# Optimization experiments

Hardware: AMD Instinct MI355X
Metric: run time of the kernel (lower is better)

Reference implementation:

```python
import jax, jax.numpy as jnp
import numpy as np

E = 256  # embedding_dim

def setup_inputs() -> dict:
    key = jax.random.key(0)
    k1, k2, k3 = jax.random.split(key, 3)
    B, P, N, D = 32, 4, 1024, E
    x = jax.random.normal(k1, (B, P, N, D), dtype=jnp.float32)
    W_qkv = jax.random.normal(k2, (D, 1 + 2 * E), dtype=jnp.float32) * (1.0 / np.sqrt(D))
    b_qkv = jnp.zeros((1 + 2 * E,), dtype=jnp.float32)
    W_o = jax.random.normal(k3, (E, E), dtype=jnp.float32) * (1.0 / np.sqrt(E))
    b_o = jnp.zeros((E,), dtype=jnp.float32)
    return {"x": x, "W_qkv": W_qkv, "b_qkv": b_qkv, "W_o": W_o, "b_o": b_o}

def reference(x, W_qkv, b_qkv, W_o, b_o):
    # qkv projection: [B,P,N,D] @ [D,1+2E] -> [B,P,N,1+2E]
    qkv = jnp.einsum('bpnd,de->bpne', x, W_qkv) + b_qkv
    q = qkv[..., :1]                 # [B,P,N,1]
    k = qkv[..., 1:1 + E]            # [B,P,N,E]
    v = jax.nn.relu(qkv[..., 1 + E:])  # [B,P,N,E]
    # softmax over patch axis N (axis=2)
    context_scores = jax.nn.softmax(q, axis=2)
    # context vector: sum over N of k * scores -> [B,P,1,E]
    context_vector = jnp.sum(k * context_scores, axis=2, keepdims=True)
    # broadcast-multiply with relu(v): [B,P,N,E] * [B,P,1,E]
    updated_values = v * context_vector
    # output projection
    out = jnp.einsum('bpnd,de->bpne', updated_values, W_o) + b_o
    return out
```

## Files before the change

### kernel.cpp

```cpp
#include <hip/hip_runtime.h>
#include <hip/hip_bf16.h>

typedef float f32x4 __attribute__((ext_vector_type(4)));
typedef short s16x8 __attribute__((ext_vector_type(8)));
typedef __bf16 bf16x8 __attribute__((ext_vector_type(8)));
typedef unsigned short u16;

#define NSEQ 1024
#define EDIM 256

#define WAITVM(N) asm volatile("s_waitcnt vmcnt(" #N ")" ::: "memory")

__device__ __forceinline__ u16 f2bf(float f){
  union { float f; unsigned u; } v; v.f = f;
  unsigned r = v.u + 0x7FFF + ((v.u >> 16) & 1);
  return (u16)(r >> 16);
}
__device__ __forceinline__ float bf2f(u16 b){
  union { float f; unsigned u; } v; v.u = ((unsigned)b) << 16;
  return v.f;
}

template <typename V>
__device__ __forceinline__ auto mfma_impl(V a, V b, f32x4 c, int)
    -> decltype(__builtin_amdgcn_mfma_f32_16x16x32_bf16(a, b, c, 0, 0, 0)) {
  return __builtin_amdgcn_mfma_f32_16x16x32_bf16(a, b, c, 0, 0, 0);
}
template <typename V>
__device__ __forceinline__ f32x4 mfma_impl(V a, V b, f32x4 c, long){
  bf16x8 ab = __builtin_bit_cast(bf16x8, a);
  bf16x8 bb = __builtin_bit_cast(bf16x8, b);
  return __builtin_amdgcn_mfma_f32_16x16x32_bf16(ab, bb, c, 0, 0, 0);
}
__device__ __forceinline__ f32x4 mfma16(s16x8 a, s16x8 b, f32x4 c){
  return mfma_impl(a, b, c, 0);
}

__device__ __forceinline__ void gload_lds16(const u16* g, u16* l){
  __builtin_amdgcn_global_load_lds((const __attribute__((address_space(1))) void*)g,
                                   (__attribute__((address_space(3))) void*)l, 16, 0, 0);
}

__global__ void k0_prep(const float* __restrict__ Wqkv, const float* __restrict__ Wo,
                        u16* __restrict__ wvf, u16* __restrict__ wof, float* __restrict__ wqc){
  int t = blockIdx.x * 256 + threadIdx.x;
  if (t < 16384){
    int which = t >> 13;
    int slot  = t & 8191;
    int l  = slot & 63;
    int nt = (slot >> 6) & 1;
    int ks = (slot >> 7) & 7;
    int c  = (slot >> 10) & 7;
    int row = ks*32 + 8*(l>>4);
    int col = c*32 + nt*16 + (l&15);
    s16x8 o8;
    if (which == 0){
      for (int j=0;j<8;j++) o8[j] = (short)f2bf(Wqkv[(size_t)(row+j)*513 + 257 + col]);
      *(s16x8*)(wvf + (size_t)slot*8) = o8;
    } else {
      for (int j=0;j<8;j++) o8[j] = (short)f2bf(Wo[(size_t)(row+j)*256 + col]);
      *(s16x8*)(wof + (size_t)slot*8) = o8;
    }
  } else if (t < 16384 + 256){
    int d = t - 16384;
    wqc[d] = Wqkv[(size_t)d*513];
  }
}

__global__ void k1_qfrag(const float* __restrict__ x, const float* __restrict__ wqc,
                         const float* __restrict__ bqkv, u16* __restrict__ xf,
                         float* __restrict__ pm, float* __restrict__ pu){
  int bp = blockIdx.x >> 6, rt = blockIdx.x & 63;
  const float* xt = x + ((size_t)bp*NSEQ + rt*16) * EDIM;
  __shared__ float xl[16][260];
  __shared__ float qs[16], es[16];
  int tid = threadIdx.x;
  for (int i=0;i<4;i++){
    int idx = tid + i*256;
    float4 vv = ((const float4*)xt)[idx];
    int row = idx >> 6, c4 = idx & 63;
    *(float4*)&xl[row][c4*4] = vv;
  }
  __syncthreads();
  int l = tid & 63, w = tid >> 6;
  int lo = l & 15, hi = l >> 4;
  for (int kk=0;kk<2;kk++){
    int ks = w*2 + kk;
    int k0 = ks*32 + 8*hi;
    s16x8 o8;
    for (int j=0;j<8;j++) o8[j] = (short)f2bf(xl[lo][k0+j]);
    size_t fo = ((((size_t)bp*64 + rt)*8 + ks)*64 + l) * 8;
    *(s16x8*)(xf + fo) = o8;
  }
  int c = l*4;
  float4 wv4 = *(const float4*)(wqc + c);
  float b0 = bqkv[0];
  for (int r=0;r<4;r++){
    int row = w*4 + r;
    float4 xv = *(float4*)&xl[row][c];
    float p = xv.x*wv4.x + xv.y*wv4.y + xv.z*wv4.z + xv.w*wv4.w;
    for (int o=32;o;o>>=1) p += __shfl_down(p, o);
    if (l == 0) qs[row] = p + b0;
  }
  __syncthreads();
  float mb = qs[0];
#pragma unroll
  for (int i=1;i<16;i++) mb = fmaxf(mb, qs[i]);
  if (tid < 16) es[tid] = expf(qs[tid] - mb);
  __syncthreads();
  float u = 0.f;
#pragma unroll
  for (int r=0;r<16;r++) u += es[r] * xl[r][tid];
  pu[(((size_t)bp*64 + rt))*256 + tid] = u;
  if (tid == 0){
    float zb = 0.f;
#pragma unroll
    for (int r=0;r<16;r++) zb += es[r];
    pm[((size_t)bp*64 + rt)*2 + 0] = mb;
    pm[((size_t)bp*64 + rt)*2 + 1] = zb;
  }
}

__global__ __launch_bounds__(512) void k34(
    const float* __restrict__ pm, const float* __restrict__ pu,
    const float* __restrict__ Wqkv, const float* __restrict__ bqkv,
    float* __restrict__ cv){
  int bp = blockIdx.x, tid = threadIdx.x;
  __shared__ float mzl[128];
  __shared__ float sf[64];
  __shared__ float tp2[2][256];
  __shared__ float tl[256];
  __shared__ float cvp[2][256];
  if (tid < 128) mzl[tid] = pm[(size_t)bp*128 + tid];
  __syncthreads();
  float M = mzl[0];
#pragma unroll
  for (int b=1;b<64;b++) M = fmaxf(M, mzl[2*b]);
  if (tid < 64) sf[tid] = expf(mzl[2*tid] - M);
  __syncthreads();
  float Z = 0.f;
#pragma unroll
  for (int b=0;b<64;b++) Z += mzl[2*b+1] * sf[b];
  float invZ = 1.0f / Z;
  int e = tid & 255, half = tid >> 8;
  float t = 0.f;
  for (int b = half*32; b < half*32 + 32; b++)
    t += pu[((size_t)bp*64 + b)*256 + e] * sf[b];
  tp2[half][e] = t;
  __syncthreads();
  if (tid < 256) tl[tid] = (tp2[0][tid] + tp2[1][tid]) * invZ;
  __syncthreads();
  float a = 0.f;
  for (int d = half*128; d < half*128 + 128; d++)
    a += tl[d] * Wqkv[(size_t)d*513 + 1 + e];
  cvp[half][e] = a;
  __syncthreads();
  if (tid < 256)
    cv[(size_t)bp*EDIM + tid] = bqkv[1 + tid] + cvp[0][tid] + cvp[1][tid];
}

__global__ __launch_bounds__(256, 2) void k5_main(
    const u16* __restrict__ xf, const u16* __restrict__ wvf, const u16* __restrict__ wof,
    const float* __restrict__ bqkv, const float* __restrict__ bo,
    const float* __restrict__ cv, float* __restrict__ out){
  int bp = blockIdx.x >> 3, rt = blockIdx.x & 7;
  int tid = threadIdx.x, l = tid & 63, w = tid >> 6;
  int lo = l & 15, hi = l >> 4;
  __shared__ u16 WBUF[2][16384];
  __shared__ u16 HB[4][16][40];

  auto stage = [&](int chunk, int buf){
    const u16* base = (chunk < 4) ? (wvf + (size_t)chunk*16384)
                                  : (wof + (size_t)(chunk-4)*16384);
    const u16* gsrc = base + (size_t)(w*8)*512 + l*8;
    u16* dst = &WBUF[buf][(size_t)(w*8)*512];
#pragma unroll
    for (int i=0;i<8;i++) gload_lds16(gsrc + i*512, dst + i*512);
  };

  stage(0, 0);

  s16x8 af0[8], af1[8];
  {
    const u16* src0 = xf + ((((size_t)bp*64 + rt*8 + 2*w + 0)*8)*64 + l)*8;
    const u16* src1 = src0 + 4096;
#pragma unroll
    for (int ks=0;ks<8;ks++){
      af0[ks] = *(const s16x8*)(src0 + (size_t)ks*512);
      af1[ks] = *(const s16x8*)(src1 + (size_t)ks*512);
    }
  }
  const float* cvb = cv + (size_t)bp*EDIM;
  float bov[4][4];
#pragma unroll
  for (int cc=0;cc<4;cc++)
#pragma unroll
    for (int qq=0;qq<4;qq++)
      bov[cc][qq] = bo[cc*64 + (qq>>1)*32 + (qq&1)*16 + lo];

  float* ob0 = out + ((size_t)bp*NSEQ + (rt*8 + 2*w + 0)*16) * EDIM;
  float* ob1 = ob0 + 16*EDIM;

  WAITVM(0);
  __builtin_amdgcn_s_barrier();
  __builtin_amdgcn_sched_barrier(0);

  s16x8 hf0[8], hf1[8];

#pragma unroll
  for (int c=0;c<8;c++){
    const int buf = c & 1;
    if (c < 7) stage(c+1, buf^1);

    f32x4 acc0[4], acc1[4];
#pragma unroll
    for (int q=0;q<4;q++){
      acc0[q] = f32x4{0.f,0.f,0.f,0.f};
      acc1[q] = f32x4{0.f,0.f,0.f,0.f};
    }

    __builtin_amdgcn_s_setprio(1);
#pragma unroll
    for (int ks=0;ks<8;ks++){
      s16x8 b[4];
#pragma unroll
      for (int q=0;q<4;q++)
        b[q] = *(const s16x8*)&WBUF[buf][(size_t)(q>>1)*8192 + (size_t)(ks*2+(q&1))*512 + l*8];
#pragma unroll
      for (int q=0;q<4;q++){
        if (c < 4){
          acc0[q] = mfma16(af0[ks], b[q], acc0[q]);
          acc1[q] = mfma16(af1[ks], b[q], acc1[q]);
        } else {
          acc0[q] = mfma16(hf0[ks], b[q], acc0[q]);
          acc1[q] = mfma16(hf1[ks], b[q], acc1[q]);
        }
      }
    }
    __builtin_amdgcn_s_setprio(0);

    if (c < 4){
#pragma unroll
      for (int rs=0;rs<2;rs++){
#pragma unroll
        for (int s=0;s<2;s++){
          int colA = c*64 + s*32 + lo, colB = colA + 16;
          float bvA = bqkv[257 + colA], bvB = bqkv[257 + colB];
          float csA = cvb[colA],        csB = cvb[colB];
#pragma unroll
          for (int r=0;r<4;r++){
            float hA = (rs ? acc1[s*2][r]   : acc0[s*2][r])   + bvA;
            float hB = (rs ? acc1[s*2+1][r] : acc0[s*2+1][r]) + bvB;
            HB[w][hi*4 + r][lo]      = f2bf(hA > 0.f ? hA*csA : 0.f);
            HB[w][hi*4 + r][16 + lo] = f2bf(hB > 0.f ? hB*csB : 0.f);
          }
          if (rs == 0) hf0[2*c + s] = *(const s16x8*)&HB[w][lo][8*hi];
          else         hf1[2*c + s] = *(const s16x8*)&HB[w][lo][8*hi];
        }
      }
    } else {
      int c2 = c - 4;
#pragma unroll
      for (int s=0;s<2;s++){
        int colA = c2*64 + s*32 + lo;
#pragma unroll
        for (int r=0;r<4;r++){
          size_t ro = (size_t)(hi*4 + r)*EDIM;
          ob0[ro + colA]      = acc0[s*2][r]   + bov[c2][s*2];
          ob0[ro + colA + 16] = acc0[s*2+1][r] + bov[c2][s*2+1];
          ob1[ro + colA]      = acc1[s*2][r]   + bov[c2][s*2];
          ob1[ro + colA + 16] = acc1[s*2+1][r] + bov[c2][s*2+1];
        }
      }
    }

    if (c < 7){
      if (c < 4) WAITVM(0); else WAITVM(32);
      __builtin_amdgcn_s_barrier();
      __builtin_amdgcn_sched_barrier(0);
    }
  }
}

extern "C" void kernel_launch(void* const* d_in, const int* in_sizes, int n_in,
                              void* d_out, int out_size, void* d_ws, size_t ws_size,
                              hipStream_t stream){
  const float* x    = (const float*)d_in[0];
  const float* Wqkv = (const float*)d_in[1];
  const float* bqkv = (const float*)d_in[2];
  const float* Wo   = (const float*)d_in[3];
  const float* bo   = (const float*)d_in[4];
  float* out = (float*)d_out;
  char* ws = (char*)d_ws;
  u16*   xf  = (u16*)(ws);
  u16*   wvf = (u16*)(ws + 67108864);
  u16*   wof = (u16*)(ws + 67239936);
  float* pm  = (float*)(ws + 67371008);
  float* pu  = (float*)(ws + 67436544);
  float* cvv = (float*)(ws + 75825152);
  float* wqc = (float*)(ws + 75956224);

  hipLaunchKernelGGL(k0_prep,  dim3(65),   dim3(256), 0, stream, Wqkv, Wo, wvf, wof, wqc);
  hipLaunchKernelGGL(k1_qfrag, dim3(8192), dim3(256), 0, stream, x, wqc, bqkv, xf, pm, pu);
  hipLaunchKernelGGL(k34,      dim3(128),  dim3(512), 0, stream, pm, pu, Wqkv, bqkv, cvv);
  hipLaunchKernelGGL(k5_main,  dim3(1024), dim3(256), 0, stream, xf, wvf, wof, bqkv, bo, cvv, out);
}
```

Before: 119.0 us.

## Read weight fragments directly from global memory instead of LDS double-buffering

Removes the shared-memory double-buffered staging of the pre-swizzled weight chunks (global_load_lds plus barriers). Each wave now loads its B fragments directly from global/L2 in 16 smaller column chunks. This drops the 64KB LDS buffer and all the block-wide barriers, which should help occupancy and cut synchronisation. In exchange every wave issues redundant global loads of the same weights and loses the explicit prefetch overlap.

```diff
diff --git a/kernel.cpp b/kernel.cpp
--- a/kernel.cpp
+++ b/kernel.cpp
@@ -8,8 +8,6 @@
 
 #define NSEQ 1024
 #define EDIM 256
-
-#define WAITVM(N) asm volatile("s_waitcnt vmcnt(" #N ")" ::: "memory")
 
 __device__ __forceinline__ u16 f2bf(float f){
   union { float f; unsigned u; } v; v.f = f;
@@ -34,11 +32,6 @@
 }
 __device__ __forceinline__ f32x4 mfma16(s16x8 a, s16x8 b, f32x4 c){
   return mfma_impl(a, b, c, 0);
-}
-
-__device__ __forceinline__ void gload_lds16(const u16* g, u16* l){
-  __builtin_amdgcn_global_load_lds((const __attribute__((address_space(1))) void*)g,
-                                   (__attribute__((address_space(3))) void*)l, 16, 0, 0);
 }
 
 __global__ void k0_prep(const float* __restrict__ Wqkv, const float* __restrict__ Wo,
@@ -166,19 +159,7 @@
   int bp = blockIdx.x >> 3, rt = blockIdx.x & 7;
   int tid = threadIdx.x, l = tid & 63, w = tid >> 6;
   int lo = l & 15, hi = l >> 4;
-  __shared__ u16 WBUF[2][16384];
   __shared__ u16 HB[4][16][40];
-
-  auto stage = [&](int chunk, int buf){
-    const u16* base = (chunk < 4) ? (wvf + (size_t)chunk*16384)
-                                  : (wof + (size_t)(chunk-4)*16384);
-    const u16* gsrc = base + (size_t)(w*8)*512 + l*8;
-    u16* dst = &WBUF[buf][(size_t)(w*8)*512];
-#pragma unroll
-    for (int i=0;i<8;i++) gload_lds16(gsrc + i*512, dst + i*512);
-  };
-
-  stage(0, 0);
 
   s16x8 af0[8], af1[8];
   {
@@ -191,93 +172,66 @@
     }
   }
   const float* cvb = cv + (size_t)bp*EDIM;
-  float bov[4][4];
-#pragma unroll
-  for (int cc=0;cc<4;cc++)
-#pragma unroll
-    for (int qq=0;qq<4;qq++)
-      bov[cc][qq] = bo[cc*64 + (qq>>1)*32 + (qq&1)*16 + lo];
-
   float* ob0 = out + ((size_t)bp*NSEQ + (rt*8 + 2*w + 0)*16) * EDIM;
   float* ob1 = ob0 + 16*EDIM;
 
-  WAITVM(0);
-  __builtin_amdgcn_s_barrier();
-  __builtin_amdgcn_sched_barrier(0);
-
   s16x8 hf0[8], hf1[8];
 
 #pragma unroll
-  for (int c=0;c<8;c++){
-    const int buf = c & 1;
-    if (c < 7) stage(c+1, buf^1);
-
-    f32x4 acc0[4], acc1[4];
-#pragma unroll
-    for (int q=0;q<4;q++){
-      acc0[q] = f32x4{0.f,0.f,0.f,0.f};
-      acc1[q] = f32x4{0.f,0.f,0.f,0.f};
-    }
+  for (int c=0;c<16;c++){
+    const u16* wb = ((c < 8) ? wvf : wof) + (size_t)(c & 7)*8192 + l*8;
+
+    f32x4 acc[4];
+#pragma unroll
+    for (int q=0;q<4;q++) acc[q] = f32x4{0.f,0.f,0.f,0.f};
 
     __builtin_amdgcn_s_setprio(1);
 #pragma unroll
     for (int ks=0;ks<8;ks++){
-      s16x8 b[4];
-#pragma unroll
-      for (int q=0;q<4;q++)
-        b[q] = *(const s16x8*)&WBUF[buf][(size_t)(q>>1)*8192 + (size_t)(ks*2+(q&1))*512 + l*8];
-#pragma unroll
-      for (int q=0;q<4;q++){
-        if (c < 4){
-          acc0[q] = mfma16(af0[ks], b[q], acc0[q]);
-          acc1[q] = mfma16(af1[ks], b[q], acc1[q]);
-        } else {
-          acc0[q] = mfma16(hf0[ks], b[q], acc0[q]);
-          acc1[q] = mfma16(hf1[ks], b[q], acc1[q]);
+      s16x8 b0 = *(const s16x8*)(wb + (size_t)(ks*2 + 0)*512);
+      s16x8 b1 = *(const s16x8*)(wb + (size_t)(ks*2 + 1)*512);
+      if (c < 8){
+        acc[0] = mfma16(af0[ks], b0, acc[0]);
+        acc[2] = mfma16(af1[ks], b0, acc[2]);
+        acc[1] = mfma16(af0[ks], b1, acc[1]);
+        acc[3] = mfma16(af1[ks], b1, acc[3]);
+      } else {
+        acc[0] = mfma16(hf0[ks], b0, acc[0]);
+        acc[2] = mfma16(hf1[ks], b0, acc[2]);
+        acc[1] = mfma16(hf0[ks], b1, acc[1]);
+        acc[3] = mfma16(hf1[ks], b1, acc[3]);
+      }
+    }
+    __builtin_amdgcn_s_setprio(0);
+
+    if (c < 8){
+      int colA = c*32 + lo, colB = colA + 16;
+      float bvA = bqkv[257 + colA], bvB = bqkv[257 + colB];
+      float csA = cvb[colA],        csB = cvb[colB];
+#pragma unroll
+      for (int rs=0;rs<2;rs++){
+#pragma unroll
+        for (int r=0;r<4;r++){
+          float hA = (rs ? acc[2][r] : acc[0][r]) + bvA;
+          float hB = (rs ? acc[3][r] : acc[1][r]) + bvB;
+          HB[w][hi*4 + r][lo]      = f2bf(hA > 0.f ? hA*csA : 0.f);
+          HB[w][hi*4 + r][16 + lo] = f2bf(hB > 0.f ? hB*csB : 0.f);
         }
-      }
-    }
-    __builtin_amdgcn_s_setprio(0);
-
-    if (c < 4){
-#pragma unroll
-      for (int rs=0;rs<2;rs++){
-#pragma unroll
-        for (int s=0;s<2;s++){
-          int colA = c*64 + s*32 + lo, colB = colA + 16;
-          float bvA = bqkv[257 + colA], bvB = bqkv[257 + colB];
-          float csA = cvb[colA],        csB = cvb[colB];
-#pragma unroll
-          for (int r=0;r<4;r++){
-            float hA = (rs ? acc1[s*2][r]   : acc0[s*2][r])   + bvA;
-            float hB = (rs ? acc1[s*2+1][r] : acc0[s*2+1][r]) + bvB;
-            HB[w][hi*4 + r][lo]      = f2bf(hA > 0.f ? hA*csA : 0.f);
-            HB[w][hi*4 + r][16 + lo] = f2bf(hB > 0.f ? hB*csB : 0.f);
-          }
-          if (rs == 0) hf0[2*c + s] = *(const s16x8*)&HB[w][lo][8*hi];
-          else         hf1[2*c + s] = *(const s16x8*)&HB[w][lo][8*hi];
-        }
+        if (rs == 0) hf0[c] = *(const s16x8*)&HB[w][lo][8*hi];
+        else         hf1[c] = *(const s16x8*)&HB[w][lo][8*hi];
       }
     } else {
-      int c2 = c - 4;
-#pragma unroll
-      for (int s=0;s<2;s++){
-        int colA = c2*64 + s*32 + lo;
-#pragma unroll
-        for (int r=0;r<4;r++){
-          size_t ro = (size_t)(hi*4 + r)*EDIM;
-          ob0[ro + colA]      = acc0[s*2][r]   + bov[c2][s*2];
-          ob0[ro + colA + 16] = acc0[s*2+1][r] + bov[c2][s*2+1];
-          ob1[ro + colA]      = acc1[s*2][r]   + bov[c2][s*2];
-          ob1[ro + colA + 16] = acc1[s*2+1][r] + bov[c2][s*2+1];
-        }
+      int c2 = c - 8;
+      int colA = c2*32 + lo;
+      float bbA = bo[colA], bbB = bo[colA + 16];
+#pragma unroll
+      for (int r=0;r<4;r++){
+        size_t ro = (size_t)(hi*4 + r)*EDIM;
+        ob0[ro + colA]      = acc[0][r] + bbA;
+        ob0[ro + colA + 16] = acc[1][r] + bbB;
+        ob1[ro + colA]      = acc[2][r] + bbA;
+        ob1[ro + colA + 16] = acc[3][r] + bbB;
       }
-    }
-
-    if (c < 7){
-      if (c < 4) WAITVM(0); else WAITVM(32);
-      __builtin_amdgcn_s_barrier();
-      __builtin_amdgcn_sched_barrier(0);
     }
   }
 }
```

Result: slower. 157.3 us (+32.2%).
